# Performance work log

Hardware: AMD Instinct MI355X
Metric: run time of the kernel (lower is better)

The kernel has to match this reference:

```python
import jax, jax.numpy as jnp
import numpy as np

N = 8192      # total nodes
BG = 8        # graphs in batch
NPG = 1024    # nodes per graph
DEG = 8       # in-degree per node
E = N * DEG   # edges
Q = 16        # queries per graph
D = 768       # in_dim
H = 4         # heads
F = 768       # h_feats per head
HD = H * F    # 3072


def setup_inputs() -> dict:
    key = jax.random.key(0)
    ks = jax.random.split(key, 24)
    x = jax.random.normal(ks[0], (N, D), jnp.float32)
    # block-diagonal random graph: every node has DEG incoming edges from its own graph
    edge_dst = jnp.repeat(jnp.arange(N), DEG)
    edge_src = (edge_dst // NPG) * NPG + jax.random.randint(ks[1], (E,), 0, NPG)
    query_embedding = jax.random.normal(ks[2], (BG, Q, D), jnp.float32) * 0.02
    bert_score = jax.random.uniform(ks[3], (BG, Q, NPG), jnp.float32)

    def lin(k, i, o):
        return jax.random.normal(k, (i, o), jnp.float32) * (1.0 / np.sqrt(i))

    inp = dict(x=x, edge_src=edge_src, edge_dst=edge_dst,
               query_embedding=query_embedding, bert_score=bert_score)
    inp['W1'] = lin(ks[4], D, HD)
    inp['attn_l1'] = jax.random.normal(ks[5], (H, F), jnp.float32) * 0.1
    inp['attn_r1'] = jax.random.normal(ks[6], (H, F), jnp.float32) * 0.1
    inp['b1'] = jax.random.normal(ks[7], (HD,), jnp.float32) * 0.02
    inp['gamma1'] = 1.0 + 0.1 * jax.random.normal(ks[8], (HD,), jnp.float32)
    inp['beta1'] = 0.1 * jax.random.normal(ks[9], (HD,), jnp.float32)
    inp['prelu1'] = 0.25 + 0.01 * jax.random.normal(ks[10], (HD,), jnp.float32)
    inp['W2'] = lin(ks[11], HD, HD)
    inp['attn_l2'] = jax.random.normal(ks[12], (H, F), jnp.float32) * 0.1
    inp['attn_r2'] = jax.random.normal(ks[13], (H, F), jnp.float32) * 0.1
    inp['b2'] = jax.random.normal(ks[14], (HD,), jnp.float32) * 0.02
    inp['gamma2'] = 1.0 + 0.1 * jax.random.normal(ks[15], (HD,), jnp.float32)
    inp['beta2'] = 0.1 * jax.random.normal(ks[16], (HD,), jnp.float32)
    inp['prelu2'] = 0.25 + 0.01 * jax.random.normal(ks[17], (HD,), jnp.float32)
    return inp


def _gat_layer(h, src, dst, W, al, ar, b, gamma, beta, pa):
    # DGL GATConv (eval mode, no residual): fc -> edge attention -> segment softmax -> scatter-sum
    feat = (h @ W).reshape(N, H, F)
    el = jnp.einsum('nhf,hf->nh', feat, al)            # [N,H]
    er = jnp.einsum('nhf,hf->nh', feat, ar)
    e = el[src] + er[dst]                              # [E,H]
    e = jnp.where(e > 0, e, 0.2 * e)                   # leaky_relu(0.2)
    m = jax.ops.segment_max(e, dst, num_segments=N)
    a = jnp.exp(e - m[dst])
    denom = jax.ops.segment_sum(a, dst, num_segments=N)
    alpha = a / denom[dst]                             # edge softmax over in-edges
    rst = jax.ops.segment_sum(feat[src] * alpha[:, :, None], dst, num_segments=N)
    hflat = (rst + b.reshape(1, H, F)).reshape(N, HD)
    # BatchNorm1d (training-mode batch statistics, biased var)
    mu = hflat.mean(axis=0)
    var = hflat.var(axis=0)
    hn = (hflat - mu) * jax.lax.rsqrt(var + 1e-5) * gamma + beta
    # PReLU (per-channel)
    return jnp.where(hn > 0, hn, pa * hn)


def _lambda_mrr(y_pred, y_true):
    # y_pred/y_true: [Q,K]; no padding in this pipeline (y_true = 1/rank > 0)
    order = jnp.argsort(-y_pred, axis=-1)
    yp = jnp.take_along_axis(y_pred, order, axis=-1)
    yt = jnp.take_along_axis(y_true, order, axis=-1)
    mask = (yt[:, :, None] - yt[:, None, :] > 0).astype(yp.dtype)
    sdiff = jnp.clip(yp[:, :, None] - yp[:, None, :], -50.0, 50.0)
    losses = jnp.log1p(jnp.exp(-sdiff))
    return (losses * mask).sum() / mask.sum()


def _forward(x, edge_src, edge_dst, query_embedding, bert_score,
             W1, attn_l1, attn_r1, b1, gamma1, beta1, prelu1,
             W2, attn_l2, attn_r2, b2, gamma2, beta2, prelu2):
    h1 = _gat_layer(x, edge_src, edge_dst, W1, attn_l1, attn_r1, b1, gamma1, beta1, prelu1)
    m1 = h1.reshape(N, H, F).mean(axis=1)
    h2 = _gat_layer(h1, edge_src, edge_dst, W2, attn_l2, attn_r2, b2, gamma2, beta2, prelu2)
    m2 = h2.reshape(N, H, F).mean(axis=1)
    node_rep = jnp.maximum(m1, m2)                      # JumpingKnowledge(max)

    reps = node_rep.reshape(BG, NPG, F)                 # per-graph reps
    reps_flat = node_rep                                # [N,F]
    graph_of = jnp.repeat(jnp.arange(BG), NPG)          # [N]
    rank_gt = (1.0 / jnp.arange(1, NPG + 1, dtype=jnp.float32))[None, :]  # [1,K]

    def per_graph(i, rep_i, q, bs):
        order = jnp.argsort(-bs, axis=-1)               # [Q,NPG] bert rank (desc)
        p = rep_i[order[:, 0]]                          # [Q,F] positive
        neg = rep_i[order[:, 1:]]                       # [Q,NPG-1,F] own negatives
        p_sim = jnp.sum(q * p, axis=-1, keepdims=True)  # [Q,1]
        own_sim = jnp.einsum('qf,qkf->qk', q, neg)      # [Q,NPG-1]
        all_sim = q @ reps_flat.T                       # [Q,N] for in-batch negatives
        other = (graph_of != i).astype(q.dtype)         # mask out own graph
        rank_pred = jnp.concatenate([p_sim, own_sim], axis=-1)  # first K cols of ranking_list
        mrr = _lambda_mrr(rank_pred, jnp.broadcast_to(rank_gt, rank_pred.shape))
        pe = jnp.exp(p_sim).sum(axis=-1)
        ne = jnp.exp(own_sim).sum(axis=-1) + (jnp.exp(all_sim) * other).sum(axis=-1)
        cl = jnp.mean(-jnp.log(pe / (pe + ne)))
        logp = jax.nn.log_softmax(q @ rep_i.T, axis=-1)
        ent = jnp.mean(-(jnp.exp(logp) * logp).sum(axis=-1))
        return cl, mrr, ent

    cl_g, mrr_g, ent_g = jax.vmap(per_graph)(jnp.arange(BG), reps, query_embedding, bert_score)
    return cl_g.mean(), mrr_g.mean(), ent_g.mean()


def reference(x, edge_src, edge_dst, query_embedding, bert_score,
              W1, attn_l1, attn_r1, b1, gamma1, beta1, prelu1,
              W2, attn_l2, attn_r2, b2, gamma2, beta2, prelu2):
    return _forward(x, edge_src, edge_dst, query_embedding, bert_score,
                    W1, attn_l1, attn_r1, b1, gamma1, beta1, prelu1,
                    W2, attn_l2, attn_r2, b2, gamma2, beta2, prelu2)
```

## Files before the change

kernel.cpp:

```cpp
#include <hip/hip_runtime.h>
#include <hip/hip_bf16.h>
#include <hip/hip_fp16.h>

#define NN 8192
#define DD 768
#define HH 4
#define FF 768
#define HD 3072
#define BGr 8
#define NPGr 1024
#define QQ 16
#define NQ 128
#define DEGr 8
#define MRR_SPLIT 64
#define WSCALE 32.0f
#define WSCALE_INV 0.03125f

typedef __attribute__((ext_vector_type(8))) short bf16x8;
typedef __attribute__((ext_vector_type(4))) float f32x4;
typedef __attribute__((ext_vector_type(4))) int i32x4;
typedef __attribute__((ext_vector_type(8))) int i32x8;

__device__ __forceinline__ unsigned short f2bf(float f) {
    union { float f; unsigned u; } v; v.f = f;
    unsigned u = v.u;
    unsigned r = (u + 0x7fffu + ((u >> 16) & 1u)) >> 16;
    return (unsigned short)r;
}
__device__ __forceinline__ float bf2f(unsigned short u) {
    union { unsigned u; float f; } v; v.u = ((unsigned)u) << 16;
    return v.f;
}
__device__ __forceinline__ unsigned char f2fp8(float x) {
    unsigned s = (__float_as_uint(x) >> 24) & 0x80;
    __half h = __float2half(fabsf(x) * 0.00390625f);
    unsigned t = (unsigned)__half_as_ushort(h);
    t += 0x3F + ((t >> 7) & 1);
    unsigned b = t >> 7;
    if (b > 0x7E) b = 0x7E;
    return (unsigned char)(s | b);
}
__device__ __forceinline__ float fp82f(unsigned u) {
    unsigned short hb = (unsigned short)(((u & 0x80) << 8) | ((u & 0x7F) << 7));
    return __half2float(__ushort_as_half(hb)) * 256.f;
}

__device__ __forceinline__ void gl_lds16(const void* g, void* l) {
    __builtin_amdgcn_global_load_lds(
        (const __attribute__((address_space(1))) unsigned int*)g,
        (__attribute__((address_space(3))) unsigned int*)l, 16, 0, 0);
}

#define PB_Z 13
#define PB_CX (PB_Z + 6144)
#define PB_CQ (PB_CX + 96)
#define PB_T1 (PB_CQ + 2304)
#define PB_T2 (PB_T1 + 9216)
__global__ __launch_bounds__(256) void prep_k(const float* __restrict__ x,
                                              unsigned char* __restrict__ xb,
                                              const float* __restrict__ qe,
                                              unsigned short* __restrict__ qeb,
                                              const float* __restrict__ W1,
                                              unsigned char* __restrict__ w1t,
                                              const float* __restrict__ W2,
                                              unsigned char* __restrict__ w2t,
                                              float* __restrict__ stats1,
                                              float* __restrict__ stats2,
                                              float* __restrict__ out) {
    __shared__ float tile[32][33];
    int blk = blockIdx.x, tid = threadIdx.x;
    if (blk < PB_Z) {
        int f = blk * 1024 + tid * 4;
        if (f < 2 * HD) *(float4*)&stats1[f] = make_float4(0.f, 0.f, 0.f, 0.f);
        else if (f < 4 * HD) *(float4*)&stats2[f - 2 * HD] = make_float4(0.f, 0.f, 0.f, 0.f);
        else if (f == 4 * HD) { out[0] = 0.f; out[1] = 0.f; out[2] = 0.f; }
    } else if (blk < PB_CX) {
        int i = (blk - PB_Z) * 256 + tid;
        float4 v = ((const float4*)x)[i];
        uchar4 o;
        o.x = f2fp8(v.x); o.y = f2fp8(v.y); o.z = f2fp8(v.z); o.w = f2fp8(v.w);
        ((uchar4*)xb)[i] = o;
    } else if (blk < PB_CQ) {
        int i = (blk - PB_CX) * 256 + tid;
        float4 v = ((const float4*)qe)[i];
        ushort4 o;
        o.x = f2bf(v.x); o.y = f2bf(v.y); o.z = f2bf(v.z); o.w = f2bf(v.w);
        ((ushort4*)qeb)[i] = o;
    } else {
        const float* in; unsigned char* outp; int K, t;
        if (blk < PB_T1) { in = W1; outp = w1t; K = DD; t = blk - PB_CQ; }
        else             { in = W2; outp = w2t; K = HD; t = blk - PB_T1; }
        int n0 = (t % 96) * 32, k0 = (t / 96) * 32;
        int tx = tid & 31, ty = tid >> 5;
        #pragma unroll
        for (int i = 0; i < 4; i++) {
            int r = ty + i * 8;
            tile[r][tx] = in[(size_t)(k0 + r) * HD + n0 + tx];
        }
        __syncthreads();
        #pragma unroll
        for (int i = 0; i < 4; i++) {
            int r = ty + i * 8;
            outp[(size_t)(n0 + r) * K + k0 + tx] = f2fp8(tile[tx][r] * WSCALE);
        }
    }
}

template <bool EPI>
__global__ __launch_bounds__(256) void gemm_fp8(const unsigned char* __restrict__ A,
                                                const unsigned char* __restrict__ BT,
                                                unsigned char* __restrict__ C,
                                                float* __restrict__ elp,
                                                float* __restrict__ erp,
                                                const float* __restrict__ al,
                                                const float* __restrict__ ar,
                                                int M, int Nc, int K, float inv_scale) {
    __shared__ __align__(16) unsigned char As[128 * 128];
    __shared__ __align__(16) unsigned char Bs[128 * 128];
    int tid = threadIdx.x;
    int m0 = blockIdx.x * 128;
    int n0 = blockIdx.y * 128;
    int w = tid >> 6, lane = tid & 63;
    int wr = w >> 1, wc = w & 1;
    int lm = lane & 15, lq = lane >> 4;

    f32x4 acc[4][4] = {};

    int srow = tid >> 3, su = tid & 7;
    const unsigned char* Ag[4];
    const unsigned char* Bg[4];
    unsigned char* AsW[4];
    unsigned char* BsW[4];
    #pragma unroll
    for (int s = 0; s < 4; s++) {
        int row = srow + 32 * s;
        int uu = su ^ (row & 7);
        Ag[s]  = A  + (size_t)(m0 + row) * K + uu * 16;
        Bg[s]  = BT + (size_t)(n0 + row) * K + uu * 16;
        AsW[s] = &As[row * 128 + su * 16];
        BsW[s] = &Bs[row * 128 + su * 16];
    }

    for (int k0 = 0; k0 < K; k0 += 128) {
        __syncthreads();
        #pragma unroll
        for (int s = 0; s < 4; s++) {
            gl_lds16(Ag[s], AsW[s]);
            gl_lds16(Bg[s], BsW[s]);
        }
        __syncthreads();

        i32x8 af[4];
        #pragma unroll
        for (int i = 0; i < 4; i++) {
            int row = wr * 64 + i * 16 + lm;
            int sw = (row & 7) << 4;
            i32x4 lo = *(const i32x4*)&As[row * 128 + ((lq * 32) ^ sw)];
            i32x4 hi = *(const i32x4*)&As[row * 128 + ((lq * 32 + 16) ^ sw)];
            i32x8 v;
            v[0] = lo[0]; v[1] = lo[1]; v[2] = lo[2]; v[3] = lo[3];
            v[4] = hi[0]; v[5] = hi[1]; v[6] = hi[2]; v[7] = hi[3];
            af[i] = v;
        }
        #pragma unroll
        for (int j = 0; j < 4; j++) {
            int row = wc * 64 + j * 16 + lm;
            int sw = (row & 7) << 4;
            i32x4 lo = *(const i32x4*)&Bs[row * 128 + ((lq * 32) ^ sw)];
            i32x4 hi = *(const i32x4*)&Bs[row * 128 + ((lq * 32 + 16) ^ sw)];
            i32x8 bv;
            bv[0] = lo[0]; bv[1] = lo[1]; bv[2] = lo[2]; bv[3] = lo[3];
            bv[4] = hi[0]; bv[5] = hi[1]; bv[6] = hi[2]; bv[7] = hi[3];
            #pragma unroll
            for (int i = 0; i < 4; i++)
                acc[i][j] = __builtin_amdgcn_mfma_scale_f32_16x16x128_f8f6f4(
                    af[i], bv, acc[i][j], 0, 0, 0, 127, 0, 127);
        }

        #pragma unroll
        for (int s = 0; s < 4; s++) { Ag[s] += 128; Bg[s] += 128; }
    }

    #pragma unroll
    for (int i = 0; i < 4; i++)
        #pragma unroll
        for (int j = 0; j < 4; j++)
            #pragma unroll
            for (int r = 0; r < 4; r++)
                acc[i][j][r] *= inv_scale;

    #pragma unroll
    for (int i = 0; i < 4; i++) {
        int row = m0 + wr * 64 + i * 16 + lq * 4;
        #pragma unroll
        for (int j = 0; j < 4; j++) {
            int col = n0 + wc * 64 + j * 16 + lm;
            #pragma unroll
            for (int r = 0; r < 4; r++)
                C[(size_t)(row + r) * Nc + col] = f2fp8(acc[i][j][r]);
        }
    }

    if (EPI) {
        int h = n0 / FF;
        int cb = (n0 % FF) >> 7;
        float alv[4], arv[4];
        #pragma unroll
        for (int j = 0; j < 4; j++) {
            int col = n0 + wc * 64 + j * 16 + lm;
            alv[j] = al[col];
            arv[j] = ar[col];
        }
        #pragma unroll
        for (int i = 0; i < 4; i++) {
            #pragma unroll
            for (int r = 0; r < 4; r++) {
                float se = acc[i][0][r] * alv[0] + acc[i][1][r] * alv[1]
                         + acc[i][2][r] * alv[2] + acc[i][3][r] * alv[3];
                float sr_ = acc[i][0][r] * arv[0] + acc[i][1][r] * arv[1]
                          + acc[i][2][r] * arv[2] + acc[i][3][r] * arv[3];
                #pragma unroll
                for (int mm = 1; mm <= 8; mm <<= 1) {
                    se  += __shfl_xor(se, mm, 64);
                    sr_ += __shfl_xor(sr_, mm, 64);
                }
                if (lm == 0) {
                    int row = m0 + wr * 64 + i * 16 + lq * 4 + r;
                    size_t slot = ((size_t)row * HH + h) * 12 + cb * 2 + wc;
                    elp[slot] = se;
                    erp[slot] = sr_;
                }
            }
        }
    }
}

__global__ __launch_bounds__(256) void gemm_bt(const unsigned short* __restrict__ A,
                                               const unsigned short* __restrict__ BT,
                                               float* __restrict__ Ct,
                                               int M, int Nc, int K) {
    __shared__ unsigned short As[128 * 64];
    __shared__ unsigned short Bs[128 * 64];
    int tid = threadIdx.x;
    int m0 = blockIdx.x * 128;
    int n0 = blockIdx.y * 128;
    int w = tid >> 6, lane = tid & 63;
    int wr = w >> 1, wc = w & 1;
    int lm = lane & 15, lq = lane >> 4;

    f32x4 acc[4][4] = {};

    int pc = tid & 7;
    const unsigned short* Ag[4];
    const unsigned short* Bg[4];
    unsigned short* AsW[4];
    unsigned short* BsW[4];
    #pragma unroll
    for (int s = 0; s < 4; s++) {
        int row = (tid >> 3) + 32 * s;
        int lc = pc ^ (row & 7);
        Ag[s]  = A  + (size_t)(m0 + row) * K + lc * 8;
        Bg[s]  = BT + (size_t)(n0 + row) * K + lc * 8;
        AsW[s] = &As[(row * 8 + pc) * 8];
        BsW[s] = &Bs[(row * 8 + pc) * 8];
    }

    for (int k0 = 0; k0 < K; k0 += 64) {
        __syncthreads();
        #pragma unroll
        for (int s = 0; s < 4; s++) {
            gl_lds16(Ag[s], AsW[s]);
            gl_lds16(Bg[s], BsW[s]);
        }
        __syncthreads();

        #pragma unroll
        for (int kk = 0; kk < 2; kk++) {
            bf16x8 af[4], bfr[4];
            #pragma unroll
            for (int i = 0; i < 4; i++) {
                int row = wr * 64 + i * 16 + lm;
                int phys = (kk * 4 + lq) ^ (row & 7);
                af[i] = *(const bf16x8*)&As[row * 64 + phys * 8];
            }
            #pragma unroll
            for (int j = 0; j < 4; j++) {
                int row = wc * 64 + j * 16 + lm;
                int phys = (kk * 4 + lq) ^ (row & 7);
                bfr[j] = *(const bf16x8*)&Bs[row * 64 + phys * 8];
            }
            #pragma unroll
            for (int i = 0; i < 4; i++)
                #pragma unroll
                for (int j = 0; j < 4; j++)
                    acc[i][j] = __builtin_amdgcn_mfma_f32_16x16x32_bf16(af[i], bfr[j], acc[i][j], 0, 0, 0);
        }

        #pragma unroll
        for (int s = 0; s < 4; s++) { Ag[s] += 64; Bg[s] += 64; }
    }

    #pragma unroll
    for (int i = 0; i < 4; i++) {
        int row = m0 + wr * 64 + i * 16 + lq * 4;
        #pragma unroll
        for (int j = 0; j < 4; j++) {
            int col = n0 + wc * 64 + j * 16 + lm;
            float4 o = make_float4(acc[i][j][0], acc[i][j][1], acc[i][j][2], acc[i][j][3]);
            *(float4*)&Ct[(size_t)col * M + row] = o;
        }
    }
}

__global__ __launch_bounds__(384) void aggregate_k(const unsigned char* __restrict__ feat,
                                                   const float* __restrict__ elp,
                                                   const float* __restrict__ erp,
                                                   const int* __restrict__ esrc,
                                                   const float* __restrict__ bias,
                                                   unsigned short* __restrict__ out) {
    int b = blockIdx.x;
    int nbase = (b & 7) * NPGr + (b >> 3) * 8;
    int t = threadIdx.x;
    __shared__ int s_src[8][DEGr];
    __shared__ float s_el[8][DEGr][HH];
    __shared__ float s_er[8][HH];
    __shared__ float s_alpha[8][DEGr][HH];
    if (t < 64) s_src[t >> 3][t & 7] = esrc[(size_t)(nbase + (t >> 3)) * DEGr + (t & 7)];
    __syncthreads();
    if (t < 256) {
        int nd = t >> 5, k = (t >> 2) & 7, h = t & 3;
        const float* pp = &elp[((size_t)s_src[nd][k] * HH + h) * 12];
        float s = 0.f;
        #pragma unroll
        for (int q = 0; q < 12; q++) s += pp[q];
        s_el[nd][k][h] = s;
    }
    if (t < 32) {
        int nd = t >> 2, h = t & 3;
        const float* pp = &erp[((size_t)(nbase + nd) * HH + h) * 12];
        float s = 0.f;
        #pragma unroll
        for (int q = 0; q < 12; q++) s += pp[q];
        s_er[nd][h] = s;
    }
    __syncthreads();
    if (t < 32) {
        int nd = t >> 2, h = t & 3;
        float e[DEGr], m = -1e30f;
        #pragma unroll
        for (int k = 0; k < DEGr; k++) {
            float v = s_el[nd][k][h] + s_er[nd][h];
            v = v > 0.f ? v : 0.2f * v;
            e[k] = v; m = fmaxf(m, v);
        }
        float d = 0.f;
        #pragma unroll
        for (int k = 0; k < DEGr; k++) { e[k] = __expf(e[k] - m); d += e[k]; }
        float inv = 1.0f / d;
        #pragma unroll
        for (int k = 0; k < DEGr; k++) s_alpha[nd][k][h] = e[k] * inv;
    }
    __syncthreads();

    int c8 = t * 8;
    int h = t / 96;
    float4 b0 = *(const float4*)&bias[c8];
    float4 b1 = *(const float4*)&bias[c8 + 4];
    float bb[8] = {b0.x, b0.y, b0.z, b0.w, b1.x, b1.y, b1.z, b1.w};
    #pragma unroll
    for (int nd = 0; nd < 8; nd++) {
        float a[8] = {bb[0], bb[1], bb[2], bb[3], bb[4], bb[5], bb[6], bb[7]};
        #pragma unroll
        for (int k = 0; k < DEGr; k++) {
            float wv = s_alpha[nd][k][h];
            unsigned long fv = *(const unsigned long*)&feat[(size_t)s_src[nd][k] * HD + c8];
            #pragma unroll
            for (int e = 0; e < 8; e++)
                a[e] += wv * fp82f((unsigned)((fv >> (8 * e)) & 0xFF));
        }
        union { unsigned short u[8]; bf16x8 v; } o;
        #pragma unroll
        for (int e = 0; e < 8; e++) o.u[e] = f2bf(a[e]);
        *(bf16x8*)&out[(size_t)(nbase + nd) * HD + c8] = o.v;
    }
}

__global__ __launch_bounds__(256) void ln_stats_k(const unsigned short* __restrict__ x,
                                                  float* __restrict__ sums) {
    int col = (blockIdx.x * 256 + threadIdx.x) * 4;
    int r0 = blockIdx.y * 128;
    float s[4] = {0.f, 0.f, 0.f, 0.f}, s2[4] = {0.f, 0.f, 0.f, 0.f};
    for (int r = r0; r < r0 + 128; r++) {
        ushort4 v = *(const ushort4*)&x[(size_t)r * HD + col];
        float f0 = bf2f(v.x), f1 = bf2f(v.y), f2 = bf2f(v.z), f3 = bf2f(v.w);
        s[0] += f0; s[1] += f1; s[2] += f2; s[3] += f3;
        s2[0] += f0 * f0; s2[1] += f1 * f1; s2[2] += f2 * f2; s2[3] += f3 * f3;
    }
    #pragma unroll
    for (int e = 0; e < 4; e++) {
        atomicAdd(&sums[col + e], s[e]);
        atomicAdd(&sums[HD + col + e], s2[e]);
    }
}

__device__ __forceinline__ void ln_vals(const unsigned short* __restrict__ x, int n, int col,
                                        const float* __restrict__ sums,
                                        const float* __restrict__ gamma,
                                        const float* __restrict__ beta,
                                        const float* __restrict__ prelu,
                                        float* val) {
    const float invN = 1.0f / (float)NN;
    ushort4 v = *(const ushort4*)&x[(size_t)n * HD + col];
    float4 sm = *(const float4*)&sums[col];
    float4 sq = *(const float4*)&sums[HD + col];
    float4 g = *(const float4*)&gamma[col];
    float4 b = *(const float4*)&beta[col];
    float4 p = *(const float4*)&prelu[col];
    float vv[4] = {bf2f(v.x), bf2f(v.y), bf2f(v.z), bf2f(v.w)};
    float ss[4] = {sm.x, sm.y, sm.z, sm.w};
    float qq[4] = {sq.x, sq.y, sq.z, sq.w};
    float gg[4] = {g.x, g.y, g.z, g.w};
    float bb[4] = {b.x, b.y, b.z, b.w};
    float pp[4] = {p.x, p.y, p.z, p.w};
    #pragma unroll
    for (int e = 0; e < 4; e++) {
        float mu = ss[e] * invN;
        float var = qq[e] * invN - mu * mu;
        float rs = rsqrtf(var + 1e-5f);
        float t = (vv[e] - mu) * rs * gg[e] + bb[e];
        val[e] = t > 0.f ? t : pp[e] * t;
    }
}

__global__ __launch_bounds__(192) void ln_norm_mean_k(const unsigned short* __restrict__ x,
                                                      const float* __restrict__ sums,
                                                      const float* __restrict__ gamma,
                                                      const float* __restrict__ beta,
                                                      const float* __restrict__ prelu,
                                                      unsigned char* __restrict__ h,
                                                      unsigned short* __restrict__ m1) {
    int n = blockIdx.x, tid = threadIdx.x;
    int c = tid * 4;
    float acc4[4] = {0.f, 0.f, 0.f, 0.f};
    #pragma unroll
    for (int hh = 0; hh < HH; hh++) {
        int col = hh * FF + c;
        float val[4];
        ln_vals(x, n, col, sums, gamma, beta, prelu, val);
        uchar4 o;
        o.x = f2fp8(val[0]); o.y = f2fp8(val[1]); o.z = f2fp8(val[2]); o.w = f2fp8(val[3]);
        *(uchar4*)&h[(size_t)n * HD + col] = o;
        #pragma unroll
        for (int e = 0; e < 4; e++) acc4[e] += val[e];
    }
    ushort4 o;
    o.x = f2bf(0.25f * acc4[0]); o.y = f2bf(0.25f * acc4[1]);
    o.z = f2bf(0.25f * acc4[2]); o.w = f2bf(0.25f * acc4[3]);
    *(ushort4*)&m1[(size_t)n * FF + c] = o;
}

__global__ __launch_bounds__(192) void ln_norm_rep_k(const unsigned short* __restrict__ x,
                                                     const float* __restrict__ sums,
                                                     const float* __restrict__ gamma,
                                                     const float* __restrict__ beta,
                                                     const float* __restrict__ prelu,
                                                     const unsigned short* __restrict__ m1,
                                                     unsigned short* __restrict__ rep) {
    int n = blockIdx.x, tid = threadIdx.x;
    int c = tid * 4;
    float acc4[4] = {0.f, 0.f, 0.f, 0.f};
    #pragma unroll
    for (int hh = 0; hh < HH; hh++) {
        int col = hh * FF + c;
        float val[4];
        ln_vals(x, n, col, sums, gamma, beta, prelu, val);
        #pragma unroll
        for (int e = 0; e < 4; e++) acc4[e] += val[e];
    }
    ushort4 m = *(const ushort4*)&m1[(size_t)n * FF + c];
    ushort4 o;
    o.x = f2bf(fmaxf(bf2f(m.x), 0.25f * acc4[0]));
    o.y = f2bf(fmaxf(bf2f(m.y), 0.25f * acc4[1]));
    o.z = f2bf(fmaxf(bf2f(m.z), 0.25f * acc4[2]));
    o.w = f2bf(fmaxf(bf2f(m.w), 0.25f * acc4[3]));
    *(ushort4*)&rep[(size_t)n * FF + c] = o;
}

__global__ __launch_bounds__(256) void loss_k(const float* __restrict__ simsQ,
                                              const float* __restrict__ bert,
                                              float* __restrict__ out) {
    __shared__ float y[NPGr];
    __shared__ float bs[NPGr];
    __shared__ float red[256];
    __shared__ int redi[256];
    int tid = threadIdx.x;

    if (blockIdx.x < NQ * MRR_SPLIT) {
        int qq = blockIdx.x >> 6;
        int sp = blockIdx.x & (MRR_SPLIT - 1);
        int g = qq >> 4;
        #pragma unroll
        for (int i = 0; i < 4; i++) {
            int idx = tid + 256 * i;
            y[idx]  = simsQ[(size_t)qq * NN + g * NPGr + idx];
            bs[idx] = bert[(size_t)qq * NPGr + idx];
        }
        __syncthreads();
        const float L2E = 1.44269504f;
        float s = 0.f;
        #pragma unroll
        for (int t = 0; t < 8; t++) {
            int rows[2] = { sp * 8 + t, 1023 - (sp * 8 + t) };
            #pragma unroll
            for (int u = 0; u < 2; u++) {
                int a = rows[u];
                float ya = y[a], ba = bs[a];
                for (int b = a + 1 + tid; b < NPGr; b += 256) {
                    float d = (bs[b] > ba) ? (ya - y[b]) : (y[b] - ya);
                    float xv = fminf(fmaxf(d, -50.f), 50.f);
                    s += __builtin_amdgcn_logf(1.0f + __builtin_amdgcn_exp2f(xv * L2E));
                }
            }
        }
        red[tid] = s; __syncthreads();
        for (int o = 128; o; o >>= 1) { if (tid < o) red[tid] += red[tid + o]; __syncthreads(); }
        if (tid == 0)
            atomicAdd(&out[1], red[0] * (0.69314718f / (523776.0f * (float)NQ)));
    } else {
        int qq = blockIdx.x - NQ * MRR_SPLIT;
        int g = qq >> 4;
        const float* S = simsQ + (size_t)qq * NN;
        const float* Sg = S + g * NPGr;
        float m = -1e30f;
        for (int n = tid; n < NN; n += 256) m = fmaxf(m, S[n]);
        red[tid] = m; __syncthreads();
        for (int o = 128; o; o >>= 1) { if (tid < o) red[tid] = fmaxf(red[tid], red[tid + o]); __syncthreads(); }
        float mAll = red[0]; __syncthreads();
        float mg = -1e30f;
        for (int j = tid; j < NPGr; j += 256) mg = fmaxf(mg, Sg[j]);
        red[tid] = mg; __syncthreads();
        for (int o = 128; o; o >>= 1) { if (tid < o) red[tid] = fmaxf(red[tid], red[tid + o]); __syncthreads(); }
        float mG = red[0]; __syncthreads();
        float z = 0.f;
        for (int n = tid; n < NN; n += 256) z += __expf(S[n] - mAll);
        red[tid] = z; __syncthreads();
        for (int o = 128; o; o >>= 1) { if (tid < o) red[tid] += red[tid + o]; __syncthreads(); }
        float Zall = red[0]; __syncthreads();
        float zg = 0.f, tg = 0.f;
        for (int j = tid; j < NPGr; j += 256) {
            float s = Sg[j];
            float e = __expf(s - mG);
            zg += e; tg += e * s;
        }
        red[tid] = zg; __syncthreads();
        for (int o = 128; o; o >>= 1) { if (tid < o) red[tid] += red[tid + o]; __syncthreads(); }
        float Zg = red[0]; __syncthreads();
        red[tid] = tg; __syncthreads();
        for (int o = 128; o; o >>= 1) { if (tid < o) red[tid] += red[tid + o]; __syncthreads(); }
        float Tg = red[0]; __syncthreads();
        float bb = -1e30f; int bi = NPGr;
        for (int j = tid; j < NPGr; j += 256) {
            float v = bert[(size_t)qq * NPGr + j];
            if (v > bb) { bb = v; bi = j; }
        }
        red[tid] = bb; redi[tid] = bi; __syncthreads();
        for (int o = 128; o; o >>= 1) {
            if (tid < o) {
                if (red[tid + o] > red[tid] || (red[tid + o] == red[tid] && redi[tid + o] < redi[tid])) {
                    red[tid] = red[tid + o]; redi[tid] = redi[tid + o];
                }
            }
            __syncthreads();
        }
        if (tid == 0) {
            float p_sim = Sg[redi[0]];
            float lse = mAll + logf(Zall);
            atomicAdd(&out[0], (lse - p_sim) * (1.0f / (float)NQ));
            float entv = (mG + logf(Zg)) - Tg / Zg;
            atomicAdd(&out[2], entv * (1.0f / (float)NQ));
        }
    }
}

extern "C" void kernel_launch(void* const* d_in, const int* in_sizes, int n_in,
                              void* d_out, int out_size, void* d_ws, size_t ws_size,
                              hipStream_t stream) {
    const float* x    = (const float*)d_in[0];
    const int* esrc   = (const int*)d_in[1];
    const float* qe   = (const float*)d_in[3];
    const float* bert = (const float*)d_in[4];
    const float* W1   = (const float*)d_in[5];
    const float* al1  = (const float*)d_in[6];
    const float* ar1  = (const float*)d_in[7];
    const float* b1   = (const float*)d_in[8];
    const float* g1   = (const float*)d_in[9];
    const float* be1  = (const float*)d_in[10];
    const float* p1   = (const float*)d_in[11];
    const float* W2   = (const float*)d_in[12];
    const float* al2  = (const float*)d_in[13];
    const float* ar2  = (const float*)d_in[14];
    const float* b2   = (const float*)d_in[15];
    const float* g2   = (const float*)d_in[16];
    const float* be2  = (const float*)d_in[17];
    const float* p2   = (const float*)d_in[18];
    float* out = (float*)d_out;
    (void)in_sizes; (void)n_in; (void)out_size; (void)ws_size;

    char* p = (char*)d_ws;
    auto alloc = [&](size_t bytes) -> void* {
        void* r = (void*)p;
        p += (bytes + 255) & ~(size_t)255;
        return r;
    };
    unsigned char*  featB = (unsigned char*)alloc((size_t)NN * HD);
    unsigned short* hflat = (unsigned short*)alloc((size_t)NN * HD * 2);
    unsigned char*  hbuf  = (unsigned char*)alloc((size_t)NN * HD);
    unsigned short* repb  = (unsigned short*)alloc((size_t)NN * FF * 2);
    unsigned char*  w1t   = (unsigned char*)alloc((size_t)HD * DD);
    unsigned char*  w2t   = (unsigned char*)alloc((size_t)HD * HD);
    unsigned short* m1    = (unsigned short*)alloc((size_t)NN * FF * 2);
    float* elp            = (float*)alloc((size_t)NN * HH * 12 * 4);
    float* erp            = (float*)alloc((size_t)NN * HH * 12 * 4);
    unsigned short* qeb   = (unsigned short*)alloc((size_t)NQ * FF * 2);
    float* simsQ          = (float*)alloc((size_t)NQ * NN * 4);
    float* stats1         = (float*)alloc((size_t)2 * HD * 4);
    float* stats2         = (float*)alloc((size_t)2 * HD * 4);
    unsigned char* xb     = (unsigned char*)repb;

    prep_k<<<PB_T2, 256, 0, stream>>>(x, xb, qe, qeb, W1, w1t, W2, w2t, stats1, stats2, out);

    gemm_fp8<true><<<dim3(NN / 128, HD / 128), 256, 0, stream>>>(
        xb, w1t, featB, elp, erp, al1, ar1, NN, HD, DD, WSCALE_INV);
    aggregate_k<<<NN / 8, 384, 0, stream>>>(featB, elp, erp, esrc, b1, hflat);
    ln_stats_k<<<dim3(HD / 1024, NN / 128), 256, 0, stream>>>(hflat, stats1);
    ln_norm_mean_k<<<NN, 192, 0, stream>>>(hflat, stats1, g1, be1, p1, hbuf, m1);

    gemm_fp8<true><<<dim3(NN / 128, HD / 128), 256, 0, stream>>>(
        hbuf, w2t, featB, elp, erp, al2, ar2, NN, HD, HD, WSCALE_INV);
    aggregate_k<<<NN / 8, 384, 0, stream>>>(featB, elp, erp, esrc, b2, hflat);
    ln_stats_k<<<dim3(HD / 1024, NN / 128), 256, 0, stream>>>(hflat, stats2);
    ln_norm_rep_k<<<NN, 192, 0, stream>>>(hflat, stats2, g2, be2, p2, m1, repb);

    gemm_bt<<<dim3(NN / 128, 1), 256, 0, stream>>>(repb, qeb, simsQ, NN, NQ, FF);

    loss_k<<<NQ * MRR_SPLIT + NQ, 256, 0, stream>>>(simsQ, bert, out);
}
```

Baseline: 590.2 us.

## Tile pairwise MRR loss into upper-triangular 128x128 blocks per query

The pairwise ranking loss now splits each query's 1024x1024 upper-triangular pair set into 36 tiles of 128x128, one block per tile. Before, each of 64 blocks per query reloaded the full 1024-entry score and bert arrays and walked rows with strided, unevenly sized inner loops. Now each block loads only its two 128-element slices and every thread runs a fixed 64-iteration loop. This cuts redundant global loads and block count. Diagonal tiles compute masked-out lower-triangle terms, which adds some wasted transcendental work.

Result: faster. 547.4 us (-7.3%).

```diff
diff --git a/kernel.cpp b/kernel.cpp
--- a/kernel.cpp
+++ b/kernel.cpp
@@ -12,7 +12,7 @@
 #define QQ 16
 #define NQ 128
 #define DEGr 8
-#define MRR_SPLIT 64
+#define MRR_TILES 36
 #define WSCALE 32.0f
 #define WSCALE_INV 0.03125f
 
@@ -489,37 +489,54 @@
 __global__ __launch_bounds__(256) void loss_k(const float* __restrict__ simsQ,
                                               const float* __restrict__ bert,
                                               float* __restrict__ out) {
-    __shared__ float y[NPGr];
-    __shared__ float bs[NPGr];
+    __shared__ float s_ya[128];
+    __shared__ float s_ba[128];
     __shared__ float red[256];
     __shared__ int redi[256];
     int tid = threadIdx.x;
 
-    if (blockIdx.x < NQ * MRR_SPLIT) {
-        int qq = blockIdx.x >> 6;
-        int sp = blockIdx.x & (MRR_SPLIT - 1);
+    if (blockIdx.x < NQ * MRR_TILES) {
+        int qq = blockIdx.x / MRR_TILES;
+        int t36 = blockIdx.x % MRR_TILES;
+        int I = 0, rem = t36;
+        while (rem >= 8 - I) { rem -= 8 - I; I++; }
+        int J = I + rem;
         int g = qq >> 4;
-        #pragma unroll
-        for (int i = 0; i < 4; i++) {
-            int idx = tid + 256 * i;
-            y[idx]  = simsQ[(size_t)qq * NN + g * NPGr + idx];
-            bs[idx] = bert[(size_t)qq * NPGr + idx];
-        }
+        const float* Y = simsQ + (size_t)qq * NN + (size_t)g * NPGr;
+        const float* B = bert + (size_t)qq * NPGr;
+        int a0 = I * 128, b0 = J * 128;
+
+        if (tid < 128) s_ya[tid] = Y[a0 + tid];
+        else           s_ba[tid - 128] = B[a0 + (tid - 128)];
+        int bl = tid & 127;
+        int bcol = b0 + bl;
+        float yb = Y[bcol];
+        float bbv = B[bcol];
         __syncthreads();
+
         const float L2E = 1.44269504f;
+        int abase = (tid >> 7) * 64;
         float s = 0.f;
-        #pragma unroll
-        for (int t = 0; t < 8; t++) {
-            int rows[2] = { sp * 8 + t, 1023 - (sp * 8 + t) };
-            #pragma unroll
-            for (int u = 0; u < 2; u++) {
-                int a = rows[u];
-                float ya = y[a], ba = bs[a];
-                for (int b = a + 1 + tid; b < NPGr; b += 256) {
-                    float d = (bs[b] > ba) ? (ya - y[b]) : (y[b] - ya);
-                    float xv = fminf(fmaxf(d, -50.f), 50.f);
-                    s += __builtin_amdgcn_logf(1.0f + __builtin_amdgcn_exp2f(xv * L2E));
-                }
+        if (I == J) {
+            #pragma unroll 4
+            for (int ai = 0; ai < 64; ai++) {
+                int a = abase + ai;
+                float ya = s_ya[a], ba = s_ba[a];
+                float tdf = ya - yb;
+                float d = (bbv > ba) ? tdf : -tdf;
+                float xv = fminf(fmaxf(d, -50.f), 50.f);
+                float term = __builtin_amdgcn_logf(1.0f + __builtin_amdgcn_exp2f(xv * L2E));
+                s += (bl > a) ? term : 0.f;
+            }
+        } else {
+            #pragma unroll 4
+            for (int ai = 0; ai < 64; ai++) {
+                int a = abase + ai;
+                float ya = s_ya[a], ba = s_ba[a];
+                float tdf = ya - yb;
+                float d = (bbv > ba) ? tdf : -tdf;
+                float xv = fminf(fmaxf(d, -50.f), 50.f);
+                s += __builtin_amdgcn_logf(1.0f + __builtin_amdgcn_exp2f(xv * L2E));
             }
         }
         red[tid] = s; __syncthreads();
@@ -527,7 +544,7 @@
         if (tid == 0)
             atomicAdd(&out[1], red[0] * (0.69314718f / (523776.0f * (float)NQ)));
     } else {
-        int qq = blockIdx.x - NQ * MRR_SPLIT;
+        int qq = blockIdx.x - NQ * MRR_TILES;
         int g = qq >> 4;
         const float* S = simsQ + (size_t)qq * NN;
         const float* Sg = S + g * NPGr;
@@ -643,5 +660,5 @@
 
     gemm_bt<<<dim3(NN / 128, 1), 256, 0, stream>>>(repb, qeb, simsQ, NN, NQ, FF);
 
-    loss_k<<<NQ * MRR_SPLIT + NQ, 256, 0, stream>>>(simsQ, bert, out);
-}
+    loss_k<<<NQ * MRR_TILES + NQ, 256, 0, stream>>>(simsQ, bert, out);
+}
```
